# Kernel optimization log

Hardware: AMD Instinct MI355X
Metric: run time of the kernel (lower is better)

Reference implementation:

```python
import jax, jax.numpy as jnp
import numpy as np

V, E, HS, HT, L = 128, 256, 512, 512, 2  # vocab, emb, src_hidden, tgt_hidden, layers
T, B, S = 32, 128, 128                   # tgt steps, batch, src len


def _lstm_cell(x, h, c, Wih, Whh, bih, bhh):
    g = x @ Wih.T + bih + h @ Whh.T + bhh
    i, f, gg, o = jnp.split(g, 4, axis=-1)  # torch LSTMCell gate order i,f,g,o
    i, f, o = jax.nn.sigmoid(i), jax.nn.sigmoid(f), jax.nn.sigmoid(o)
    c2 = f * c + i * jnp.tanh(gg)
    return o * jnp.tanh(c2), c2


def setup_inputs() -> dict:
    key = jax.random.key(0)
    ks = jax.random.split(key, 20)
    s = 0.05
    inp = {
        "sot_id": 1,
        "target": jax.random.randint(ks[0], (T, B), 0, V),
        "src_emb": jax.random.normal(ks[1], (S, B, E), jnp.float32),
        "src_outputs": jax.random.normal(ks[2], (S, B, HS), jnp.float32),
        "mask_src": jnp.ones((S, B), bool),
        "h0": jax.random.normal(ks[3], (L, B, HT), jnp.float32) * s,
        "c0": jax.random.normal(ks[4], (L, B, HT), jnp.float32) * s,
        "emb_weight": jax.random.normal(ks[5], (V, E), jnp.float32) * s,
        "W_ih0": jax.random.normal(ks[6], (4 * HT, E), jnp.float32) * s,
        "W_hh0": jax.random.normal(ks[7], (4 * HT, HT), jnp.float32) * s,
        "b_ih0": jnp.zeros((4 * HT,), jnp.float32),
        "b_hh0": jnp.zeros((4 * HT,), jnp.float32),
        "W_ih1": jax.random.normal(ks[8], (4 * HT, HT), jnp.float32) * s,
        "W_hh1": jax.random.normal(ks[9], (4 * HT, HT), jnp.float32) * s,
        "b_ih1": jnp.zeros((4 * HT,), jnp.float32),
        "b_hh1": jnp.zeros((4 * HT,), jnp.float32),
        "Wa": jax.random.normal(ks[10], (HS, HT), jnp.float32) * s,
        "W_hidden": jax.random.normal(ks[11], (E, HS + HT), jnp.float32) * s,
        "b_hidden": jnp.zeros((E,), jnp.float32),
    }
    return inp


def reference(sot_id, target, src_emb, src_outputs, mask_src, h0, c0,
              emb_weight, W_ih0, W_hh0, b_ih0, b_hh0, W_ih1, W_hh1, b_ih1, b_hh1,
              Wa, W_hidden, b_hidden):
    # Wh_s does not depend on the decode step: hoist (same math, one GEMM).
    Wh_s = jnp.einsum('sbd,dt->sbt', src_outputs, Wa)  # [S,B,HT]
    neg = jnp.float32(-9999.9)
    ratio = jnp.float32(0.2)  # norms_or_ratios = [1.0, 0.2], relative control

    # teacher forcing: step 0 uses sot_id, then target[:-1]
    toks = jnp.concatenate([jnp.full((1, B), sot_id, target.dtype), target[:-1]], axis=0)

    def step(carry, tok):
        h, c = carry  # [L,B,HT]
        x = emb_weight[tok]  # [B,E]
        h0n, c0n = _lstm_cell(x, h[0], c[0], W_ih0, W_hh0, b_ih0, b_hh0)
        h1n, c1n = _lstm_cell(h0n, h[1], c[1], W_ih1, W_hh1, b_ih1, b_hh1)
        ht = h1n  # top-layer hidden [B,HT]
        scores = jnp.sum(Wh_s * ht[None], axis=-1)          # [S,B]
        scores = jnp.where(mask_src, scores, neg)
        almt = jax.nn.softmax(scores, axis=0)               # log_softmax(0).exp()
        ctx = jnp.einsum('sb,sbd->bd', almt, src_outputs)   # [B,HS]
        hid_cat = jnp.concatenate([ht, ctx], axis=-1) @ W_hidden.T + b_hidden  # [B,E]
        ctx_emb = jnp.einsum('sb,sbe->be', almt, src_emb)   # [B,E]
        # NormControlledResidual, relative mode
        norm_base = jnp.linalg.norm(ctx_emb, axis=-1, keepdims=True)
        norm_act = jnp.linalg.norm(hid_cat, axis=-1, keepdims=True)
        adj = jnp.minimum(norm_act, norm_base * ratio)
        hid_res = ctx_emb + hid_cat / jnp.maximum(norm_act, 1e-12) * adj
        log_prob = jax.nn.log_softmax(hid_res @ emb_weight.T, axis=-1)  # [B,V]
        return (jnp.stack([h0n, h1n]), jnp.stack([c0n, c1n])), log_prob

    _, log_probs = jax.lax.scan(step, (h0, c0), toks)
    return log_probs  # [T,B,V]
```

## Files before the change

### kernel.cpp

```cpp
#include <hip/hip_runtime.h>
#include <hip/hip_bf16.h>
#include <cstdint>
#include <cstddef>

constexpr int cV = 128, cE = 256, cHS = 512, cHT = 512;
constexpr int cT = 32, cB = 128, cS = 128;
constexpr int NP = 128, NBLK = 256, NTHR = 256;
constexpr int NC = 127;
constexpr int HB = cB * cHT;
constexpr int NCTR = cT + 1;

typedef float f32x4 __attribute__((ext_vector_type(4)));
typedef short bf16x8 __attribute__((ext_vector_type(8)));
#define MFMA16(a, b, c) __builtin_amdgcn_mfma_f32_16x16x32_bf16((a), (b), (c), 0, 0, 0)

struct SyncS {
  int pflags[NP];
  int cflags[NP];
  int prel;   int pad1[31];
  int crel;   int pad2[31];
  int csetup; int pad3[31];
  int texit;  int pad4[31];
  int dflag[NP * 32];
  int drelp[NP * 32];
  int drelc[NCTR * 32];
  int bnext[cB * 32];
};
__device__ __align__(128) SyncS gs;

struct KParams {
  const int* sot; const int* target;
  const float* src_emb; const float* src_out;
  const float* h0in; const float* c0in;
  const float* emb;
  const float* Wih0; const float* Whh0; const float* bih0; const float* bhh0;
  const float* Wih1; const float* Whh1; const float* bih1; const float* bhh1;
  const float* Wa; const float* Wh; const float* bh;
  float* out;
  float* XW0b;
  float* b1sum;
  unsigned short* h0init;
  unsigned short* h0hist;
  unsigned short* h1hist;
  unsigned short* WaT;
  unsigned short* Wh_bf;
  unsigned short* emb_bf;
  unsigned short* WhS;
  unsigned short* soT;
  unsigned short* embT;
};

__device__ __forceinline__ unsigned short f2bf(float f) {
  __hip_bfloat16 h = __float2bfloat16(f);
  unsigned short u; __builtin_memcpy(&u, &h, 2); return u;
}
__device__ __forceinline__ void bf8dec(uint4 r, float* o) {
  o[0] = __uint_as_float(r.x << 16); o[1] = __uint_as_float(r.x & 0xffff0000u);
  o[2] = __uint_as_float(r.y << 16); o[3] = __uint_as_float(r.y & 0xffff0000u);
  o[4] = __uint_as_float(r.z << 16); o[5] = __uint_as_float(r.z & 0xffff0000u);
  o[6] = __uint_as_float(r.w << 16); o[7] = __uint_as_float(r.w & 0xffff0000u);
}
__device__ __forceinline__ uint4 pack8(const float* f) {
  uint4 r;
  r.x = f2bf(f[0]) | ((unsigned)f2bf(f[1]) << 16);
  r.y = f2bf(f[2]) | ((unsigned)f2bf(f[3]) << 16);
  r.z = f2bf(f[4]) | ((unsigned)f2bf(f[5]) << 16);
  r.w = f2bf(f[6]) | ((unsigned)f2bf(f[7]) << 16);
  return r;
}
__device__ __forceinline__ float sigmoidf_(float x) { return 1.0f / (1.0f + __expf(-x)); }
__device__ __forceinline__ float tanhf_(float x) {
  return 1.0f - 2.0f / (__expf(2.0f * x) + 1.0f);
}

__device__ __forceinline__ void st_co64(void* p, unsigned long long v) {
  __hip_atomic_store((unsigned long long*)p, v, __ATOMIC_RELAXED, __HIP_MEMORY_SCOPE_AGENT);
}
__device__ __forceinline__ int ld_rx(const int* p) {
  return __hip_atomic_load(p, __ATOMIC_RELAXED, __HIP_MEMORY_SCOPE_AGENT);
}
__device__ __forceinline__ void st_rx(int* p, int v) {
  __hip_atomic_store(p, v, __ATOMIC_RELAXED, __HIP_MEMORY_SCOPE_AGENT);
}

__device__ __forceinline__ void group_bar(int* flags, int* rel, int me, bool lead,
                                          int round, int tid) {
  __syncthreads();
  if (tid == 0)
    __hip_atomic_store(&flags[me], round, __ATOMIC_RELEASE, __HIP_MEMORY_SCOPE_AGENT);
  if (lead) {
    if (tid < 64) {
      for (;;) {
        int a = ld_rx(&flags[tid]);
        int b = ld_rx(&flags[tid + 64]);
        if (__all(a >= round && b >= round)) break;
        __builtin_amdgcn_s_sleep(1);
      }
      if (tid == 0) {
        (void)__hip_atomic_load(&flags[0], __ATOMIC_ACQUIRE, __HIP_MEMORY_SCOPE_AGENT);
        __hip_atomic_store(rel, round, __ATOMIC_RELEASE, __HIP_MEMORY_SCOPE_AGENT);
      }
    }
  } else if (tid == 0) {
    while (ld_rx(rel) < round) __builtin_amdgcn_s_sleep(1);
    (void)__hip_atomic_load(rel, __ATOMIC_ACQUIRE, __HIP_MEMORY_SCOPE_AGENT);
  }
  __syncthreads();
}

__device__ __forceinline__ void group_bar127(int* flags, int* rel, int me, bool lead,
                                             int round, int tid) {
  __syncthreads();
  if (tid == 0)
    __hip_atomic_store(&flags[me], round, __ATOMIC_RELEASE, __HIP_MEMORY_SCOPE_AGENT);
  if (lead) {
    if (tid < 64) {
      for (;;) {
        int a = ld_rx(&flags[tid]);
        int b = ld_rx(&flags[tid + 63]);
        if (__all(a >= round && b >= round)) break;
        __builtin_amdgcn_s_sleep(1);
      }
      if (tid == 0) {
        (void)__hip_atomic_load(&flags[0], __ATOMIC_ACQUIRE, __HIP_MEMORY_SCOPE_AGENT);
        __hip_atomic_store(rel, round, __ATOMIC_RELEASE, __HIP_MEMORY_SCOPE_AGENT);
      }
    }
  } else if (tid == 0) {
    while (ld_rx(rel) < round) __builtin_amdgcn_s_sleep(1);
    (void)__hip_atomic_load(rel, __ATOMIC_ACQUIRE, __HIP_MEMORY_SCOPE_AGENT);
  }
  __syncthreads();
}

__device__ __forceinline__ float block_red_max(float v, float* red) {
  #pragma unroll
  for (int o = 1; o < 64; o <<= 1) v = fmaxf(v, __shfl_xor(v, o));
  if ((threadIdx.x & 63) == 0) red[threadIdx.x >> 6] = v;
  __syncthreads();
  float r = fmaxf(fmaxf(red[0], red[1]), fmaxf(red[2], red[3]));
  __syncthreads();
  return r;
}
__device__ __forceinline__ float block_red_sum(float v, float* red) {
  #pragma unroll
  for (int o = 1; o < 64; o <<= 1) v += __shfl_xor(v, o);
  if ((threadIdx.x & 63) == 0) red[threadIdx.x >> 6] = v;
  __syncthreads();
  float r = red[0] + red[1] + red[2] + red[3];
  __syncthreads();
  return r;
}

__device__ __forceinline__ void cell2(const KParams& p, f32x4 acc, int layer, int t,
                                      int mtg, float* cr, unsigned* hstageL,
                                      int ub, int n16, int quad, int sot0) {
  float vf[4], vg[4], vo[4];
  #pragma unroll
  for (int r = 0; r < 4; ++r) {
    vf[r] = __shfl_xor(acc[r], 4);
    vg[r] = __shfl_xor(acc[r], 8);
    vo[r] = __shfl_xor(acc[r], 12);
  }
  if (n16 < 4) {
    const int u = ub + n16;
    const int brow = mtg * 16 + quad * 4;
    float4 xq[4];
    if (layer == 0) {
      if (t == 0) {
        float4 x = *(const float4*)(p.XW0b + ((size_t)sot0 * 512 + u) * 4);
        xq[0] = xq[1] = xq[2] = xq[3] = x;
      } else {
        const int* tr = p.target + (t - 1) * cB + brow;
        #pragma unroll
        for (int r = 0; r < 4; ++r)
          xq[r] = *(const float4*)(p.XW0b + ((size_t)tr[r] * 512 + u) * 4);
      }
    } else {
      float4 x = *(const float4*)(p.b1sum + (size_t)u * 4);
      xq[0] = xq[1] = xq[2] = xq[3] = x;
    }
    #pragma unroll
    for (int r = 0; r < 4; ++r) {
      float i_ = sigmoidf_(acc[r] + xq[r].x);
      float f_ = sigmoidf_(vf[r] + xq[r].y);
      float g_ = tanhf_(vg[r] + xq[r].z);
      float o_ = sigmoidf_(vo[r] + xq[r].w);
      float c2 = f_ * cr[r] + i_ * g_;
      cr[r] = c2;
      unsigned mine = (unsigned)f2bf(o_ * tanhf_(c2));
      unsigned partner = (unsigned)__shfl_xor((int)mine, 1);
      if ((n16 & 1) == 0)
        hstageL[(brow + r) * 2 + (n16 >> 1)] = mine | (partner << 16);
    }
  }
}

__global__ __launch_bounds__(NTHR, 1) void lstm_attn_decoder(KParams p) {
  __shared__ __align__(16) unsigned char smem[51264];
  const int tid = threadIdx.x;
  const int blk = blockIdx.x;
  const int lane = tid & 63, wv = tid >> 6;
  const int n16 = lane & 15, quad = lane >> 4;
  float* fsm = (float*)smem;
  unsigned* hstage = (unsigned*)(smem + 49152);
  int* task_slot = (int*)(smem + 51200);

  if (blk < NP) {
    const int pgid = blk * NTHR + tid, pstr = NP * NTHR;
    for (int i = pgid; i < 2048; i += pstr)
      p.b1sum[i] = p.bih1[(i & 3) * 512 + (i >> 2)] + p.bhh1[(i & 3) * 512 + (i >> 2)];
    for (int i = pgid; i < HB; i += pstr) {
      int b = i >> 9, u = i & 511;
      int dst = (u >> 3) * 1024 + b * 8 + (u & 7);
      p.h0init[dst] = f2bf(p.h0in[i]);
      p.h1hist[dst] = f2bf(p.h0in[HB + i]);
    }
    {
      int vt = blk >> 4, jt = blk & 15;
      #pragma unroll
      for (int i = 0; i < 4; ++i) {
        int f4 = tid + NTHR * i;
        int r = f4 >> 6, c4 = f4 & 63;
        ((float4*)fsm)[f4] = ((const float4*)(p.emb + (size_t)(vt * 16 + r) * cE))[c4];
      }
      __syncthreads();
      int j = jt * 128 + (tid & 127), vh = tid >> 7;
      float acc[8] = {0,0,0,0,0,0,0,0};
      const float4* wr = (const float4*)(p.Wih0 + (size_t)j * cE);
      for (int k4 = 0; k4 < 64; ++k4) {
        float4 w4 = wr[k4];
        #pragma unroll
        for (int vv = 0; vv < 8; ++vv) {
          float4 ev = ((const float4*)fsm)[(vh * 8 + vv) * 64 + k4];
          acc[vv] = fmaf(w4.x, ev.x, fmaf(w4.y, ev.y, fmaf(w4.z, ev.z, fmaf(w4.w, ev.w, acc[vv]))));
        }
      }
      float bj = p.bih0[j] + p.bhh0[j];
      int gate = j >> 9, u = j & 511;
      #pragma unroll
      for (int vv = 0; vv < 8; ++vv)
        p.XW0b[((size_t)(vt * 16 + vh * 8 + vv) * 512 + u) * 4 + gate] = acc[vv] + bj;
      __syncthreads();
    }
    const int ub = blk * 4;
    for (int g = tid; g < 3072; g += NTHR) {
      int mat = g >> 10, rem = g & 1023, n = rem >> 6, kg = rem & 63;
      const float* Wsrc = mat == 0 ? p.Whh0 : (mat == 1 ? p.Wih1 : p.Whh1);
      int grow = (n >> 2) * 512 + ub + (n & 3);
      const float4* src = (const float4*)(Wsrc + (size_t)grow * cHT + kg * 8);
      float4 x0 = src[0], x1 = src[1];
      float tmp[8] = {x0.x, x0.y, x0.z, x0.w, x1.x, x1.y, x1.z, x1.w};
      *(uint4*)(smem + mat * 16384 + (kg >> 2) * 1024 + ((kg & 3) * 16 + n) * 16) = pack8(tmp);
    }
    float creg[2][2][4];
    {
      const int uc = ub + (n16 & 3);
      #pragma unroll
      for (int l = 0; l < 2; ++l)
        #pragma unroll
        for (int i2 = 0; i2 < 2; ++i2) {
          int brow = (wv * 2 + i2) * 16 + quad * 4;
          #pragma unroll
          for (int r = 0; r < 4; ++r)
            creg[l][i2][r] = p.c0in[(size_t)l * HB + (size_t)(brow + r) * cHT + uc];
        }
    }
    group_bar(gs.pflags, &gs.prel, blk, blk == 0, 1, tid);

    const int sot0 = p.sot[0];
    const int rp_blk = blk >> 1, half = blk & 1;
    const int brow0 = (wv * 2 + 0) * 16 + n16;
    const int brow1 = (wv * 2 + 1) * 16 + n16;
    for (int k = 0; k <= cT; ++k) {
      if (k >= 1) {
        if (tid == 0) {
          while (ld_rx(&gs.drelp[blk * 32]) < k) __builtin_amdgcn_s_sleep(1);
          asm volatile("" ::: "memory");
        }
        __syncthreads();
      }
      const unsigned short* A0p = (k == 0) ? p.h0init : p.h0hist + (size_t)(k - 1) * HB;
      const unsigned short* A1p = p.h1hist + (size_t)(k >= 1 ? k - 1 : 0) * HB;
      bf16x8 fa0[16], fa1[16], fb0[16], fb1[16];
      #pragma unroll
      for (int ks = 0; ks < 16; ++ks) {
        const size_t rp = (size_t)(ks * 4 + quad) * 128;
        fa0[ks] = *(const bf16x8*)(A0p + (rp + brow0) * 8);
        fb0[ks] = *(const bf16x8*)(A0p + (rp + brow1) * 8);
      }
      if (k >= 1) {
        #pragma unroll
        for (int ks = 0; ks < 16; ++ks) {
          const size_t rp = (size_t)(ks * 4 + quad) * 128;
          fa1[ks] = *(const bf16x8*)(A1p + (rp + brow0) * 8);
          fb1[ks] = *(const bf16x8*)(A1p + (rp + brow1) * 8);
        }
      }
      __builtin_amdgcn_sched_barrier(0);
      f32x4 acc00 = {0,0,0,0}, acc01 = {0,0,0,0};
      f32x4 acc10 = {0,0,0,0}, acc11 = {0,0,0,0};
      if (k < cT) {
        #pragma unroll
        for (int ks = 0; ks < 16; ++ks) {
          const bf16x8 w = *(const bf16x8*)(smem + ks * 1024 + lane * 16);
          acc00 = MFMA16(fa0[ks], w, acc00);
          acc01 = MFMA16(fb0[ks], w, acc01);
        }
      }
      if (k >= 1) {
        #pragma unroll
        for (int ks = 0; ks < 16; ++ks) {
          const bf16x8 w = *(const bf16x8*)(smem + 16384 + ks * 1024 + lane * 16);
          acc10 = MFMA16(fa0[ks], w, acc10);
          acc11 = MFMA16(fb0[ks], w, acc11);
        }
        #pragma unroll
        for (int ks = 0; ks < 16; ++ks) {
          const bf16x8 w = *(const bf16x8*)(smem + 32768 + ks * 1024 + lane * 16);
          acc10 = MFMA16(fa1[ks], w, acc10);
          acc11 = MFMA16(fb1[ks], w, acc11);
        }
      }
      if (k < cT) {
        cell2(p, acc00, 0, k, wv * 2 + 0, creg[0][0], hstage, ub, n16, quad, sot0);
        cell2(p, acc01, 0, k, wv * 2 + 1, creg[0][1], hstage, ub, n16, quad, sot0);
      }
      if (k >= 1) {
        cell2(p, acc10, 1, k - 1, wv * 2 + 0, creg[1][0], hstage + 256, ub, n16, quad, sot0);
        cell2(p, acc11, 1, k - 1, wv * 2 + 1, creg[1][1], hstage + 256, ub, n16, quad, sot0);
      }
      __syncthreads();
      if (wv == 0) {
        if (k < cT) {
          uint4 v = *(const uint4*)((const unsigned char*)hstage + lane * 16);
          unsigned short* d = p.h0hist + (size_t)k * HB + rp_blk * 1024 + lane * 16 + half * 4;
          st_co64(d, (unsigned long long)v.x | ((unsigned long long)v.y << 32));
          st_co64(d + 8, (unsigned long long)v.z | ((unsigned long long)v.w << 32));
        }
        if (k >= 1) {
          uint4 v = *(const uint4*)((const unsigned char*)hstage + 1024 + lane * 16);
          unsigned short* d = p.h1hist + (size_t)k * HB + rp_blk * 1024 + lane * 16 + half * 4;
          st_co64(d, (unsigned long long)v.x | ((unsigned long long)v.y << 32));
          st_co64(d + 8, (unsigned long long)v.z | ((unsigned long long)v.w << 32));
        }
      }
      if (tid == 0) {
        asm volatile("s_waitcnt vmcnt(0)" ::: "memory");
        st_rx(&gs.dflag[blk * 32], k + 1);
      }
    }
    if (tid == 0) {
      while (!ld_rx(&gs.csetup)) __builtin_amdgcn_s_sleep(16);
      (void)__hip_atomic_load(&gs.csetup, __ATOMIC_ACQUIRE, __HIP_MEMORY_SCOPE_AGENT);
    }
    __syncthreads();
  } else if (blk == NBLK - 1) {
    if (tid < 64) {
      for (int k = 0; k <= cT; ++k) {
        for (;;) {
          int a = ld_rx(&gs.dflag[tid * 32]);
          int b = ld_rx(&gs.dflag[(tid + 64) * 32]);
          if (__all(a >= k + 1 && b >= k + 1)) break;
          __builtin_amdgcn_s_sleep(1);
        }
        asm volatile("" ::: "memory");
        st_rx(&gs.drelp[tid * 32], k + 1);
        st_rx(&gs.drelp[(tid + 64) * 32], k + 1);
        if (tid == 0) st_rx(&gs.drelc[k * 32], 1);
      }
    }
    __syncthreads();
    if (tid == 0) {
      while (!ld_rx(&gs.csetup)) __builtin_amdgcn_s_sleep(16);
      (void)__hip_atomic_load(&gs.csetup, __ATOMIC_ACQUIRE, __HIP_MEMORY_SCOPE_AGENT);
    }
    __syncthreads();
  } else {
    const int cb = blk - NP;
    const int cgid = cb * NTHR + tid, cstr = NC * NTHR;
    for (int i = cgid; i < cHT * cHS; i += cstr) {
      int t = i >> 9, d = i & 511;
      p.WaT[i] = f2bf(p.Wa[(size_t)d * cHT + t]);
    }
    for (int i = cgid; i < cE * (cHS + cHT); i += cstr) p.Wh_bf[i] = f2bf(p.Wh[i]);
    for (int i = cgid; i < cV * cE; i += cstr) p.emb_bf[i] = f2bf(p.emb[i]);
    for (int job = cb; job < 3072; job += NC) {
      int jb, d0, D; const float* src; unsigned short* dst;
      if (job < 2048) { jb = job >> 4; d0 = (job & 15) * 32; src = p.src_out; dst = p.soT;  D = cHS; }
      else { int j2 = job - 2048; jb = j2 >> 3; d0 = (j2 & 7) * 32; src = p.src_emb; dst = p.embT; D = cE; }
      int dl = tid & 31, s0 = tid >> 5;
      for (int i = 0; i < 16; ++i) {
        int s = i * 8 + s0;
        fsm[s * 33 + dl] = src[((size_t)s * cB + jb) * D + d0 + dl];
      }
      __syncthreads();
      int dl2 = tid >> 3, sb = tid & 7;
      for (int i = 0; i < 16; ++i) {
        int s = sb * 16 + i;
        dst[((size_t)jb * D + d0 + dl2) * cS + s] = f2bf(fsm[s * 33 + dl2]);
      }
      __syncthreads();
    }
    group_bar127(gs.cflags, &gs.crel, cb, cb == 0, 1, tid);
    for (int bb = cb; bb < cB; bb += NC) {
      unsigned short* stag = (unsigned short*)(smem + 17408);
      for (int mt = 0; mt < 8; ++mt) {
        bf16x8 afr[16];
        for (int hh = 0; hh < 2; ++hh) {
          __syncthreads();
          int s_loc = tid >> 4, kb = (tid & 15) * 16 + hh * 256;
          const float* src = p.src_out + (((size_t)(mt * 16 + s_loc)) * cB + bb) * cHS + kb;
          float tmp[16];
          #pragma unroll
          for (int i = 0; i < 4; ++i) {
            float4 v = ((const float4*)src)[i];
            tmp[i*4+0]=v.x; tmp[i*4+1]=v.y; tmp[i*4+2]=v.z; tmp[i*4+3]=v.w;
          }
          int ksl = (kb >> 5) - hh * 8;
          int q0 = (kb >> 3) & 3;
          *(uint4*)(stag + ((size_t)ksl * 64 + q0 * 16 + s_loc) * 8) = pack8(tmp);
          *(uint4*)(stag + ((size_t)ksl * 64 + (q0 + 1) * 16 + s_loc) * 8) = pack8(tmp + 8);
          __syncthreads();
          #pragma unroll
          for (int kk = 0; kk < 8; ++kk)
            afr[hh * 8 + kk] = *(const bf16x8*)(stag + ((size_t)kk * 64 + lane) * 8);
        }
        for (int j = 0; j < 8; ++j) {
          int nt = wv * 8 + j;
          f32x4 acc = {0.f, 0.f, 0.f, 0.f};
          const unsigned short* bp = p.WaT + ((size_t)(nt * 16 + n16)) * cHS + quad * 8;
          #pragma unroll
          for (int ks = 0; ks < 16; ++ks)
            acc = MFMA16(afr[ks], *(const bf16x8*)(bp + ks * 32), acc);
          #pragma unroll
          for (int r = 0; r < 4; ++r)
            p.WhS[((size_t)(bb * cS + mt * 16 + quad * 4 + r)) * cHT + nt * 16 + n16] = f2bf(acc[r]);
        }
      }
      __syncthreads();
    }
    group_bar127(gs.cflags, &gs.crel, cb, cb == 0, 2, tid);
    if (cb == 0 && tid == 0)
      __hip_atomic_store(&gs.csetup, 1, __ATOMIC_RELEASE, __HIP_MEMORY_SCOPE_AGENT);
  }

  {
    float* ht_s  = fsm;
    float* ctx_s = fsm + 512;
    float* ce_s  = fsm + 1024;
    float* hr_s  = fsm + 1280;
    float* sc_s  = fsm + 1536;
    float* w_s   = fsm + 1664;
    float* red   = fsm + 1792;
    float* lg_s  = fsm + 1808;

    const int b = blk & (cB - 1);
    int* bctr = &gs.bnext[b * 32];
    for (;;) {
      if (tid == 0)
        *task_slot = __hip_atomic_fetch_add(bctr, 1, __ATOMIC_RELAXED, __HIP_MEMORY_SCOPE_AGENT);
      __syncthreads();
      int t = *task_slot;
      __syncthreads();
      if (t >= cT) break;
      if (tid == 0) {
        while (ld_rx(&gs.drelc[(t + 1) * 32]) == 0) __builtin_amdgcn_s_sleep(64);
        asm volatile("" ::: "memory");
      }
      __syncthreads();
      {
        const unsigned short* hrow = p.h1hist + (size_t)(t + 1) * HB + b * 8;
        for (int i = tid; i < 64; i += NTHR) {
          uint4 r = *(const uint4*)(hrow + (size_t)i * 1024);
          float f[8]; bf8dec(r, f);
          #pragma unroll
          for (int j = 0; j < 8; ++j) ht_s[i * 8 + j] = f[j];
        }
      }
      __syncthreads();
      {
        int s = tid >> 1, hf = tid & 1;
        const uint4* r4 = (const uint4*)(p.WhS + ((size_t)(b * cS + s)) * cHT + hf * 256);
        float acc = 0;
        for (int i = 0; i < 32; ++i) {
          float f[8]; bf8dec(r4[i], f);
          #pragma unroll
          for (int jj = 0; jj < 8; ++jj) acc = fmaf(f[jj], ht_s[hf * 256 + i * 8 + jj], acc);
        }
        acc += __shfl_xor(acc, 1);
        if (hf == 0) sc_s[s] = acc;
      }
      __syncthreads();
      {
        float v = (tid < cS) ? sc_s[tid] : -3.4e38f;
        float m = block_red_max(v, red);
        float w = (tid < cS) ? __expf(sc_s[tid] - m) : 0.0f;
        float l = block_red_sum(w, red);
        if (tid < cS) w_s[tid] = w / l;
      }
      __syncthreads();
      for (int d = tid; d < cHS; d += NTHR) {
        const uint4* r4 = (const uint4*)(p.soT + ((size_t)b * cHS + d) * cS);
        float acc = 0;
        for (int i = 0; i < 16; ++i) {
          float f[8]; bf8dec(r4[i], f);
          #pragma unroll
          for (int jj = 0; jj < 8; ++jj) acc = fmaf(f[jj], w_s[i * 8 + jj], acc);
        }
        ctx_s[d] = acc;
      }
      {
        const uint4* r4 = (const uint4*)(p.embT + ((size_t)b * cE + tid) * cS);
        float acc = 0;
        for (int i = 0; i < 16; ++i) {
          float f[8]; bf8dec(r4[i], f);
          #pragma unroll
          for (int jj = 0; jj < 8; ++jj) acc = fmaf(f[jj], w_s[i * 8 + jj], acc);
        }
        ce_s[tid] = acc;
      }
      __syncthreads();
      {
        float nb2 = block_red_sum(ce_s[tid] * ce_s[tid], red);
        const uint4* r4 = (const uint4*)(p.Wh_bf + (size_t)tid * (cHS + cHT));
        float hc = p.bh[tid];
        for (int i = 0; i < 64; ++i) {
          float f[8]; bf8dec(r4[i], f);
          #pragma unroll
          for (int jj = 0; jj < 8; ++jj) hc = fmaf(f[jj], ht_s[i * 8 + jj], hc);
        }
        for (int i = 64; i < 128; ++i) {
          float f[8]; bf8dec(r4[i], f);
          #pragma unroll
          for (int jj = 0; jj < 8; ++jj) hc = fmaf(f[jj], ctx_s[(i - 64) * 8 + jj], hc);
        }
        float na2 = block_red_sum(hc * hc, red);
        float nb = sqrtf(nb2), na = sqrtf(na2);
        float adj = fminf(na, nb * 0.2f);
        float scale = adj / fmaxf(na, 1e-12f);
        hr_s[tid] = ce_s[tid] + hc * scale;
      }
      __syncthreads();
      {
        int v = tid >> 1, hf = tid & 1;
        const uint4* r4 = (const uint4*)(p.emb_bf + (size_t)v * cE + hf * 128);
        float acc = 0;
        for (int i = 0; i < 16; ++i) {
          float f[8]; bf8dec(r4[i], f);
          #pragma unroll
          for (int jj = 0; jj < 8; ++jj) acc = fmaf(f[jj], hr_s[hf * 128 + i * 8 + jj], acc);
        }
        acc += __shfl_xor(acc, 1);
        if (hf == 0) lg_s[v] = acc;
      }
      __syncthreads();
      {
        float v = (tid < cV) ? lg_s[tid] : -3.4e38f;
        float m = block_red_max(v, red);
        float w = (tid < cV) ? __expf(lg_s[tid] - m) : 0.0f;
        float l = block_red_sum(w, red);
        if (tid < cV)
          p.out[((size_t)t * cB + b) * cV + tid] = lg_s[tid] - m - logf(l);
      }
      __syncthreads();
    }
  }
  __syncthreads();
  if (tid == 0) {
    int old = __hip_atomic_fetch_add(&gs.texit, 1, __ATOMIC_ACQ_REL, __HIP_MEMORY_SCOPE_AGENT);
    if (old == NBLK - 1) {
      for (int i = 0; i < NP; ++i) {
        st_rx(&gs.pflags[i], 0);
        st_rx(&gs.cflags[i], 0);
        st_rx(&gs.dflag[i * 32], 0);
        st_rx(&gs.drelp[i * 32], 0);
      }
      for (int i = 0; i < NCTR; ++i) st_rx(&gs.drelc[i * 32], 0);
      for (int i = 0; i < cB; ++i) st_rx(&gs.bnext[i * 32], 0);
      st_rx(&gs.prel, 0); st_rx(&gs.crel, 0);
      st_rx(&gs.csetup, 0); st_rx(&gs.texit, 0);
    }
  }
}

extern "C" void kernel_launch(void* const* d_in, const int* in_sizes, int n_in,
                              void* d_out, int out_size, void* d_ws, size_t ws_size,
                              hipStream_t stream) {
  (void)in_sizes; (void)n_in; (void)out_size; (void)ws_size;
  KParams p;
  p.sot     = (const int*)d_in[0];
  p.target  = (const int*)d_in[1];
  p.src_emb = (const float*)d_in[2];
  p.src_out = (const float*)d_in[3];
  p.h0in = (const float*)d_in[5];
  p.c0in = (const float*)d_in[6];
  p.emb  = (const float*)d_in[7];
  p.Wih0 = (const float*)d_in[8];
  p.Whh0 = (const float*)d_in[9];
  p.bih0 = (const float*)d_in[10];
  p.bhh0 = (const float*)d_in[11];
  p.Wih1 = (const float*)d_in[12];
  p.Whh1 = (const float*)d_in[13];
  p.bih1 = (const float*)d_in[14];
  p.bhh1 = (const float*)d_in[15];
  p.Wa   = (const float*)d_in[16];
  p.Wh   = (const float*)d_in[17];
  p.bh   = (const float*)d_in[18];
  p.out  = (float*)d_out;

  char* base = (char*)d_ws;
  size_t off = 0;
  auto carve = [&](size_t bytes) -> void* {
    void* r = base + off;
    off += (bytes + 255) & ~(size_t)255;
    return r;
  };
  p.XW0b   = (float*)carve((size_t)cV * 2048 * 4);
  p.b1sum  = (float*)carve(2048 * 4);
  p.h0init = (unsigned short*)carve((size_t)HB * 2);
  p.h0hist = (unsigned short*)carve((size_t)cT * HB * 2);
  p.h1hist = (unsigned short*)carve((size_t)(cT + 1) * HB * 2);
  p.WaT    = (unsigned short*)carve((size_t)cHT * cHS * 2);
  p.Wh_bf  = (unsigned short*)carve((size_t)cE * (cHS + cHT) * 2);
  p.emb_bf = (unsigned short*)carve((size_t)cV * cE * 2);
  p.WhS    = (unsigned short*)carve((size_t)cB * cS * cHT * 2);
  p.soT    = (unsigned short*)carve((size_t)cB * cHS * cS * 2);
  p.embT   = (unsigned short*)carve((size_t)cB * cE * cS * 2);

  void* args[] = { (void*)&p };
  hipError_t rc = hipLaunchCooperativeKernel((const void*)lstm_attn_decoder,
                                             dim3(NBLK), dim3(NTHR), args, 0, stream);
  if (rc != hipSuccess) {
    (void)hipGetLastError();
    hipLaunchKernelGGL(lstm_attn_decoder, dim3(NBLK), dim3(NTHR), 0, stream, p);
  }
}
```

Measured before the change: 1.068 ms.

## Halve LSTM producer blocks to 64, each handling 8 hidden units

The recurrent LSTM stage moves from 128 producer blocks of 4 hidden units each to 64 blocks of 8 units. Each block now holds twice the weight slice in shared memory and issues two MFMA column tiles per fragment load, which reuses the A fragments and cuts the per-step cross-block barrier fan-in. The freed blocks become consumers (191), so each batch row gets its own block for the WhS precompute. In exchange, per-block serial work on the critical recurrent path doubles and LDS use grows to about 100 KB.

```diff
diff --git a/kernel.cpp b/kernel.cpp
--- a/kernel.cpp
+++ b/kernel.cpp
@@ -5,8 +5,8 @@
 
 constexpr int cV = 128, cE = 256, cHS = 512, cHT = 512;
 constexpr int cT = 32, cB = 128, cS = 128;
-constexpr int NP = 128, NBLK = 256, NTHR = 256;
-constexpr int NC = 127;
+constexpr int NPROD = 64, NBLK = 256, NTHR = 256;
+constexpr int NC = 191;
 constexpr int HB = cB * cHT;
 constexpr int NCTR = cT + 1;
 
@@ -15,14 +15,14 @@
 #define MFMA16(a, b, c) __builtin_amdgcn_mfma_f32_16x16x32_bf16((a), (b), (c), 0, 0, 0)
 
 struct SyncS {
-  int pflags[NP];
-  int cflags[NP];
+  int pflags[128];
+  int cflags[192];
   int prel;   int pad1[31];
   int crel;   int pad2[31];
   int csetup; int pad3[31];
   int texit;  int pad4[31];
-  int dflag[NP * 32];
-  int drelp[NP * 32];
+  int dflag[NPROD * 32];
+  int drelp[NPROD * 32];
   int drelc[NCTR * 32];
   int bnext[cB * 32];
 };
@@ -83,8 +83,8 @@
   __hip_atomic_store(p, v, __ATOMIC_RELAXED, __HIP_MEMORY_SCOPE_AGENT);
 }
 
-__device__ __forceinline__ void group_bar(int* flags, int* rel, int me, bool lead,
-                                          int round, int tid) {
+__device__ __forceinline__ void group_barN(int* flags, int* rel, int me, bool lead,
+                                           int round, int tid, int N) {
   __syncthreads();
   if (tid == 0)
     __hip_atomic_store(&flags[me], round, __ATOMIC_RELEASE, __HIP_MEMORY_SCOPE_AGENT);
@@ -92,33 +92,9 @@
     if (tid < 64) {
       for (;;) {
         int a = ld_rx(&flags[tid]);
-        int b = ld_rx(&flags[tid + 64]);
-        if (__all(a >= round && b >= round)) break;
-        __builtin_amdgcn_s_sleep(1);
-      }
-      if (tid == 0) {
-        (void)__hip_atomic_load(&flags[0], __ATOMIC_ACQUIRE, __HIP_MEMORY_SCOPE_AGENT);
-        __hip_atomic_store(rel, round, __ATOMIC_RELEASE, __HIP_MEMORY_SCOPE_AGENT);
-      }
-    }
-  } else if (tid == 0) {
-    while (ld_rx(rel) < round) __builtin_amdgcn_s_sleep(1);
-    (void)__hip_atomic_load(rel, __ATOMIC_ACQUIRE, __HIP_MEMORY_SCOPE_AGENT);
-  }
-  __syncthreads();
-}
-
-__device__ __forceinline__ void group_bar127(int* flags, int* rel, int me, bool lead,
-                                             int round, int tid) {
-  __syncthreads();
-  if (tid == 0)
-    __hip_atomic_store(&flags[me], round, __ATOMIC_RELEASE, __HIP_MEMORY_SCOPE_AGENT);
-  if (lead) {
-    if (tid < 64) {
-      for (;;) {
-        int a = ld_rx(&flags[tid]);
-        int b = ld_rx(&flags[tid + 63]);
-        if (__all(a >= round && b >= round)) break;
+        int b = (tid + 64 < N) ? ld_rx(&flags[tid + 64]) : round;
+        int c = (tid + 128 < N) ? ld_rx(&flags[tid + 128]) : round;
+        if (__all(a >= round && b >= round && c >= round)) break;
         __builtin_amdgcn_s_sleep(1);
       }
       if (tid == 0) {
@@ -153,8 +129,8 @@
 }
 
 __device__ __forceinline__ void cell2(const KParams& p, f32x4 acc, int layer, int t,
-                                      int mtg, float* cr, unsigned* hstageL,
-                                      int ub, int n16, int quad, int sot0) {
+                                      int mtg, int nt, float* cr, unsigned* hstageL,
+                                      int ub8, int n16, int quad, int sot0) {
   float vf[4], vg[4], vo[4];
   #pragma unroll
   for (int r = 0; r < 4; ++r) {
@@ -163,7 +139,7 @@
     vo[r] = __shfl_xor(acc[r], 12);
   }
   if (n16 < 4) {
-    const int u = ub + n16;
+    const int u = ub8 + nt * 4 + n16;
     const int brow = mtg * 16 + quad * 4;
     float4 xq[4];
     if (layer == 0) {
@@ -191,23 +167,23 @@
       unsigned mine = (unsigned)f2bf(o_ * tanhf_(c2));
       unsigned partner = (unsigned)__shfl_xor((int)mine, 1);
       if ((n16 & 1) == 0)
-        hstageL[(brow + r) * 2 + (n16 >> 1)] = mine | (partner << 16);
+        hstageL[(brow + r) * 4 + nt * 2 + (n16 >> 1)] = mine | (partner << 16);
     }
   }
 }
 
 __global__ __launch_bounds__(NTHR, 1) void lstm_attn_decoder(KParams p) {
-  __shared__ __align__(16) unsigned char smem[51264];
+  __shared__ __align__(16) unsigned char smem[102464];
   const int tid = threadIdx.x;
   const int blk = blockIdx.x;
   const int lane = tid & 63, wv = tid >> 6;
   const int n16 = lane & 15, quad = lane >> 4;
   float* fsm = (float*)smem;
-  unsigned* hstage = (unsigned*)(smem + 49152);
-  int* task_slot = (int*)(smem + 51200);
-
-  if (blk < NP) {
-    const int pgid = blk * NTHR + tid, pstr = NP * NTHR;
+  unsigned* hstage = (unsigned*)(smem + 98304);
+  int* task_slot = (int*)(smem + 102400);
+
+  if (blk < 128) {
+    const int pgid = blk * NTHR + tid, pstr = 128 * NTHR;
     for (int i = pgid; i < 2048; i += pstr)
       p.b1sum[i] = p.bih1[(i & 3) * 512 + (i >> 2)] + p.bhh1[(i & 3) * 512 + (i >> 2)];
     for (int i = pgid; i < HB; i += pstr) {
@@ -243,33 +219,39 @@
         p.XW0b[((size_t)(vt * 16 + vh * 8 + vv) * 512 + u) * 4 + gate] = acc[vv] + bj;
       __syncthreads();
     }
-    const int ub = blk * 4;
-    for (int g = tid; g < 3072; g += NTHR) {
-      int mat = g >> 10, rem = g & 1023, n = rem >> 6, kg = rem & 63;
+    group_barN(gs.pflags, &gs.prel, blk, blk == 0, 1, tid, 128);
+  }
+
+  if (blk < NPROD) {
+    const int ub8 = blk * 8;
+    for (int g = tid; g < 6144; g += NTHR) {
+      int mat = g >> 11, rem = g & 2047, nt = rem >> 10, r2 = rem & 1023;
+      int n = r2 >> 6, kg = r2 & 63;
       const float* Wsrc = mat == 0 ? p.Whh0 : (mat == 1 ? p.Wih1 : p.Whh1);
-      int grow = (n >> 2) * 512 + ub + (n & 3);
+      int grow = (n >> 2) * 512 + ub8 + nt * 4 + (n & 3);
       const float4* src = (const float4*)(Wsrc + (size_t)grow * cHT + kg * 8);
       float4 x0 = src[0], x1 = src[1];
       float tmp[8] = {x0.x, x0.y, x0.z, x0.w, x1.x, x1.y, x1.z, x1.w};
-      *(uint4*)(smem + mat * 16384 + (kg >> 2) * 1024 + ((kg & 3) * 16 + n) * 16) = pack8(tmp);
-    }
-    float creg[2][2][4];
+      *(uint4*)(smem + (mat * 32 + (kg >> 2) * 2 + nt) * 1024 + ((kg & 3) * 16 + n) * 16) = pack8(tmp);
+    }
+    float creg[2][2][2][4];
     {
-      const int uc = ub + (n16 & 3);
+      const int uc0 = ub8 + (n16 & 3);
       #pragma unroll
       for (int l = 0; l < 2; ++l)
         #pragma unroll
         for (int i2 = 0; i2 < 2; ++i2) {
           int brow = (wv * 2 + i2) * 16 + quad * 4;
           #pragma unroll
-          for (int r = 0; r < 4; ++r)
-            creg[l][i2][r] = p.c0in[(size_t)l * HB + (size_t)(brow + r) * cHT + uc];
-        }
-    }
-    group_bar(gs.pflags, &gs.prel, blk, blk == 0, 1, tid);
+          for (int nt = 0; nt < 2; ++nt)
+            #pragma unroll
+            for (int r = 0; r < 4; ++r)
+              creg[l][i2][nt][r] = p.c0in[(size_t)l * HB + (size_t)(brow + r) * cHT + uc0 + nt * 4];
+        }
+    }
+    __syncthreads();
 
     const int sot0 = p.sot[0];
-    const int rp_blk = blk >> 1, half = blk & 1;
     const int brow0 = (wv * 2 + 0) * 16 + n16;
     const int brow1 = (wv * 2 + 1) * 16 + n16;
     for (int k = 0; k <= cT; ++k) {
@@ -282,67 +264,76 @@
       }
       const unsigned short* A0p = (k == 0) ? p.h0init : p.h0hist + (size_t)(k - 1) * HB;
       const unsigned short* A1p = p.h1hist + (size_t)(k >= 1 ? k - 1 : 0) * HB;
-      bf16x8 fa0[16], fa1[16], fb0[16], fb1[16];
+      bf16x8 fa0[16], fb0[16], fa1[16], fb1[16];
       #pragma unroll
       for (int ks = 0; ks < 16; ++ks) {
         const size_t rp = (size_t)(ks * 4 + quad) * 128;
         fa0[ks] = *(const bf16x8*)(A0p + (rp + brow0) * 8);
         fb0[ks] = *(const bf16x8*)(A0p + (rp + brow1) * 8);
+        fa1[ks] = *(const bf16x8*)(A1p + (rp + brow0) * 8);
+        fb1[ks] = *(const bf16x8*)(A1p + (rp + brow1) * 8);
+      }
+      __builtin_amdgcn_sched_barrier(0);
+      f32x4 a000 = {0,0,0,0}, a001 = {0,0,0,0}, a010 = {0,0,0,0}, a011 = {0,0,0,0};
+      f32x4 a100 = {0,0,0,0}, a101 = {0,0,0,0}, a110 = {0,0,0,0}, a111 = {0,0,0,0};
+      if (k < cT) {
+        #pragma unroll
+        for (int ks = 0; ks < 16; ++ks) {
+          const bf16x8 w0 = *(const bf16x8*)(smem + (0 * 32 + ks * 2 + 0) * 1024 + lane * 16);
+          const bf16x8 w1 = *(const bf16x8*)(smem + (0 * 32 + ks * 2 + 1) * 1024 + lane * 16);
+          a000 = MFMA16(fa0[ks], w0, a000);
+          a001 = MFMA16(fa0[ks], w1, a001);
+          a010 = MFMA16(fb0[ks], w0, a010);
+          a011 = MFMA16(fb0[ks], w1, a011);
+        }
       }
       if (k >= 1) {
         #pragma unroll
         for (int ks = 0; ks < 16; ++ks) {
-          const size_t rp = (size_t)(ks * 4 + quad) * 128;
-          fa1[ks] = *(const bf16x8*)(A1p + (rp + brow0) * 8);
-          fb1[ks] = *(const bf16x8*)(A1p + (rp + brow1) * 8);
-        }
-      }
-      __builtin_amdgcn_sched_barrier(0);
-      f32x4 acc00 = {0,0,0,0}, acc01 = {0,0,0,0};
-      f32x4 acc10 = {0,0,0,0}, acc11 = {0,0,0,0};
-      if (k < cT) {
+          const bf16x8 w0 = *(const bf16x8*)(smem + (1 * 32 + ks * 2 + 0) * 1024 + lane * 16);
+          const bf16x8 w1 = *(const bf16x8*)(smem + (1 * 32 + ks * 2 + 1) * 1024 + lane * 16);
+          a100 = MFMA16(fa0[ks], w0, a100);
+          a101 = MFMA16(fa0[ks], w1, a101);
+          a110 = MFMA16(fb0[ks], w0, a110);
+          a111 = MFMA16(fb0[ks], w1, a111);
+        }
         #pragma unroll
         for (int ks = 0; ks < 16; ++ks) {
-          const bf16x8 w = *(const bf16x8*)(smem + ks * 1024 + lane * 16);
-          acc00 = MFMA16(fa0[ks], w, acc00);
-          acc01 = MFMA16(fb0[ks], w, acc01);
-        }
+          const bf16x8 w0 = *(const bf16x8*)(smem + (2 * 32 + ks * 2 + 0) * 1024 + lane * 16);
+          const bf16x8 w1 = *(const bf16x8*)(smem + (2 * 32 + ks * 2 + 1) * 1024 + lane * 16);
+          a100 = MFMA16(fa1[ks], w0, a100);
+          a101 = MFMA16(fa1[ks], w1, a101);
+          a110 = MFMA16(fb1[ks], w0, a110);
+          a111 = MFMA16(fb1[ks], w1, a111);
+        }
+      }
+      if (k < cT) {
+        cell2(p, a000, 0, k, wv * 2 + 0, 0, creg[0][0][0], hstage, ub8, n16, quad, sot0);
+        cell2(p, a001, 0, k, wv * 2 + 0, 1, creg[0][0][1], hstage, ub8, n16, quad, sot0);
+        cell2(p, a010, 0, k, wv * 2 + 1, 0, creg[0][1][0], hstage, ub8, n16, quad, sot0);
+        cell2(p, a011, 0, k, wv * 2 + 1, 1, creg[0][1][1], hstage, ub8, n16, quad, sot0);
       }
       if (k >= 1) {
-        #pragma unroll
-        for (int ks = 0; ks < 16; ++ks) {
-          const bf16x8 w = *(const bf16x8*)(smem + 16384 + ks * 1024 + lane * 16);
-          acc10 = MFMA16(fa0[ks], w, acc10);
-          acc11 = MFMA16(fb0[ks], w, acc11);
-        }
-        #pragma unroll
-        for (int ks = 0; ks < 16; ++ks) {
-          const bf16x8 w = *(const bf16x8*)(smem + 32768 + ks * 1024 + lane * 16);
-          acc10 = MFMA16(fa1[ks], w, acc10);
-          acc11 = MFMA16(fb1[ks], w, acc11);
-        }
-      }
-      if (k < cT) {
-        cell2(p, acc00, 0, k, wv * 2 + 0, creg[0][0], hstage, ub, n16, quad, sot0);
-        cell2(p, acc01, 0, k, wv * 2 + 1, creg[0][1], hstage, ub, n16, quad, sot0);
-      }
-      if (k >= 1) {
-        cell2(p, acc10, 1, k - 1, wv * 2 + 0, creg[1][0], hstage + 256, ub, n16, quad, sot0);
-        cell2(p, acc11, 1, k - 1, wv * 2 + 1, creg[1][1], hstage + 256, ub, n16, quad, sot0);
+        cell2(p, a100, 1, k - 1, wv * 2 + 0, 0, creg[1][0][0], hstage + 512, ub8, n16, quad, sot0);
+        cell2(p, a101, 1, k - 1, wv * 2 + 0, 1, creg[1][0][1], hstage + 512, ub8, n16, quad, sot0);
+        cell2(p, a110, 1, k - 1, wv * 2 + 1, 0, creg[1][1][0], hstage + 512, ub8, n16, quad, sot0);
+        cell2(p, a111, 1, k - 1, wv * 2 + 1, 1, creg[1][1][1], hstage + 512, ub8, n16, quad, sot0);
       }
       __syncthreads();
       if (wv == 0) {
         if (k < cT) {
-          uint4 v = *(const uint4*)((const unsigned char*)hstage + lane * 16);
-          unsigned short* d = p.h0hist + (size_t)k * HB + rp_blk * 1024 + lane * 16 + half * 4;
-          st_co64(d, (unsigned long long)v.x | ((unsigned long long)v.y << 32));
-          st_co64(d + 8, (unsigned long long)v.z | ((unsigned long long)v.w << 32));
+          const unsigned char* s = (const unsigned char*)hstage + lane * 32;
+          unsigned short* d = p.h0hist + (size_t)k * HB + (size_t)blk * 1024 + lane * 16;
+          #pragma unroll
+          for (int j = 0; j < 4; ++j)
+            st_co64(d + j * 4, *(const unsigned long long*)(s + j * 8));
         }
         if (k >= 1) {
-          uint4 v = *(const uint4*)((const unsigned char*)hstage + 1024 + lane * 16);
-          unsigned short* d = p.h1hist + (size_t)k * HB + rp_blk * 1024 + lane * 16 + half * 4;
-          st_co64(d, (unsigned long long)v.x | ((unsigned long long)v.y << 32));
-          st_co64(d + 8, (unsigned long long)v.z | ((unsigned long long)v.w << 32));
+          const unsigned char* s = (const unsigned char*)hstage + 2048 + lane * 32;
+          unsigned short* d = p.h1hist + (size_t)k * HB + (size_t)blk * 1024 + lane * 16;
+          #pragma unroll
+          for (int j = 0; j < 4; ++j)
+            st_co64(d + j * 4, *(const unsigned long long*)(s + j * 8));
         }
       }
       if (tid == 0) {
@@ -360,13 +351,11 @@
       for (int k = 0; k <= cT; ++k) {
         for (;;) {
           int a = ld_rx(&gs.dflag[tid * 32]);
-          int b = ld_rx(&gs.dflag[(tid + 64) * 32]);
-          if (__all(a >= k + 1 && b >= k + 1)) break;
+          if (__all(a >= k + 1)) break;
           __builtin_amdgcn_s_sleep(1);
         }
         asm volatile("" ::: "memory");
         st_rx(&gs.drelp[tid * 32], k + 1);
-        st_rx(&gs.drelp[(tid + 64) * 32], k + 1);
         if (tid == 0) st_rx(&gs.drelc[k * 32], 1);
       }
     }
@@ -377,7 +366,7 @@
     }
     __syncthreads();
   } else {
-    const int cb = blk - NP;
+    const int cb = blk - NPROD;
     const int cgid = cb * NTHR + tid, cstr = NC * NTHR;
     for (int i = cgid; i < cHT * cHS; i += cstr) {
       int t = i >> 9, d = i & 511;
@@ -402,15 +391,16 @@
       }
       __syncthreads();
     }
-    group_bar127(gs.cflags, &gs.crel, cb, cb == 0, 1, tid);
-    for (int bb = cb; bb < cB; bb += NC) {
+    group_barN(gs.cflags, &gs.crel, cb, cb == 0, 1, tid, NC);
+    if (cb < cB) {
+      const int b = cb;
       unsigned short* stag = (unsigned short*)(smem + 17408);
       for (int mt = 0; mt < 8; ++mt) {
         bf16x8 afr[16];
         for (int hh = 0; hh < 2; ++hh) {
           __syncthreads();
           int s_loc = tid >> 4, kb = (tid & 15) * 16 + hh * 256;
-          const float* src = p.src_out + (((size_t)(mt * 16 + s_loc)) * cB + bb) * cHS + kb;
+          const float* src = p.src_out + (((size_t)(mt * 16 + s_loc)) * cB + b) * cHS + kb;
           float tmp[16];
           #pragma unroll
           for (int i = 0; i < 4; ++i) {
@@ -435,12 +425,12 @@
             acc = MFMA16(afr[ks], *(const bf16x8*)(bp + ks * 32), acc);
           #pragma unroll
           for (int r = 0; r < 4; ++r)
-            p.WhS[((size_t)(bb * cS + mt * 16 + quad * 4 + r)) * cHT + nt * 16 + n16] = f2bf(acc[r]);
-        }
-      }
-      __syncthreads();
-    }
-    group_bar127(gs.cflags, &gs.crel, cb, cb == 0, 2, tid);
+            p.WhS[((size_t)(b * cS + mt * 16 + quad * 4 + r)) * cHT + nt * 16 + n16] = f2bf(acc[r]);
+        }
+      }
+      __syncthreads();
+    }
+    group_barN(gs.cflags, &gs.crel, cb, cb == 0, 2, tid, NC);
     if (cb == 0 && tid == 0)
       __hip_atomic_store(&gs.csetup, 1, __ATOMIC_RELEASE, __HIP_MEMORY_SCOPE_AGENT);
   }
@@ -570,9 +560,9 @@
   if (tid == 0) {
     int old = __hip_atomic_fetch_add(&gs.texit, 1, __ATOMIC_ACQ_REL, __HIP_MEMORY_SCOPE_AGENT);
     if (old == NBLK - 1) {
-      for (int i = 0; i < NP; ++i) {
-        st_rx(&gs.pflags[i], 0);
-        st_rx(&gs.cflags[i], 0);
+      for (int i = 0; i < 128; ++i) st_rx(&gs.pflags[i], 0);
+      for (int i = 0; i < 192; ++i) st_rx(&gs.cflags[i], 0);
+      for (int i = 0; i < NPROD; ++i) {
         st_rx(&gs.dflag[i * 32], 0);
         st_rx(&gs.drelp[i * 32], 0);
       }
```

Measured after the change: 1.095 ms. 2.6% more time.
